# Kernel optimization log

Measured on AMD Instinct MI355X. Metric: run time of the kernel, lower is better.

Reference implementation:

```python
import jax, jax.numpy as jnp
import numpy as np
import math

D_MODEL = 1024
NHEAD = 16
D_K = D_MODEL // NHEAD
SEQ = 2048
BATCH = 2


def setup_inputs() -> dict:
    key = jax.random.key(0)
    ks = jax.random.split(key, 8)
    s = 1.0 / math.sqrt(D_MODEL)
    return {
        "q": jax.random.normal(ks[0], (SEQ, BATCH, D_MODEL), jnp.float32),
        "k": jax.random.normal(ks[1], (SEQ, BATCH, D_MODEL), jnp.float32),
        "v": jax.random.normal(ks[2], (SEQ, BATCH, D_MODEL), jnp.float32),
        "mask": jnp.zeros((1, 1, SEQ, SEQ), jnp.float32),
        "Wq": jax.random.normal(ks[3], (D_MODEL, D_MODEL), jnp.float32) * s,
        "bq": jnp.zeros((D_MODEL,), jnp.float32),
        "Wk": jax.random.normal(ks[4], (D_MODEL, D_MODEL), jnp.float32) * s,
        "bk": jnp.zeros((D_MODEL,), jnp.float32),
        "Wv": jax.random.normal(ks[5], (D_MODEL, D_MODEL), jnp.float32) * s,
        "bv": jnp.zeros((D_MODEL,), jnp.float32),
        "Wo": jax.random.normal(ks[6], (D_MODEL, D_MODEL), jnp.float32) * s,
        "bo": jnp.zeros((D_MODEL,), jnp.float32),
    }


def _split_heads(x):
    # (seq, batch, d_model) -> (batch, nhead, seq, d_k)
    S, B, _ = x.shape
    return x.reshape(S, B, NHEAD, D_K).transpose(1, 2, 0, 3)


def reference(q, k, v, mask, Wq, bq, Wk, bk, Wv, bv, Wo, bo):
    S, B, _ = q.shape
    qh = _split_heads(q @ Wq.T + bq)  # (B, H, S, Dk)
    kh = _split_heads(k @ Wk.T + bk)
    vh = _split_heads(v @ Wv.T + bv)
    scale = 1.0 / math.sqrt(D_K)
    scores = jnp.einsum("bhsd,bhtd->bhst", qh, kh) * scale + mask
    attn = jax.nn.softmax(scores, axis=-1)  # dropout is identity at inference
    out = jnp.einsum("bhst,bhtd->bhsd", attn, vh)  # (B, H, S, Dk)
    # combine heads -> (S, B, d_model), then output projection
    out = out.transpose(2, 0, 1, 3).reshape(S, B, D_MODEL)
    return out @ Wo.T + bo
```

## Files before the change

kernel.cpp:

```cpp
#include <hip/hip_runtime.h>


#define DEV static __device__ __forceinline__

typedef unsigned short u16;
typedef __attribute__((ext_vector_type(8))) short short8;
typedef __attribute__((ext_vector_type(4))) float f32x4;
typedef __attribute__((ext_vector_type(16))) float f32x16;
typedef __attribute__((ext_vector_type(4))) unsigned short ushort4v;
typedef __attribute__((ext_vector_type(4))) unsigned int uint4v;

#define SEQ   2048
#define BATCH 2
#define DM    1024
#define NH    16
#define DKH   64
#define MROWS (SEQ*BATCH)

DEV u16 f2bf(float f) {
  union { float f; unsigned int u; } v; v.f = f;
  unsigned int u = v.u;
  return (u16)((u + 0x7FFFu + ((u >> 16) & 1u)) >> 16);
}

DEV unsigned int cvtpk_bf16(float lo, float hi) {
  unsigned int r;
  asm("v_cvt_pk_bf16_f32 %0, %1, %2" : "=v"(r) : "v"(lo), "v"(hi));
  return r;
}

DEV void permswap(unsigned int& a, unsigned int& b) {
  asm volatile("v_permlane32_swap_b32 %0, %1" : "+v"(a), "+v"(b));
}

#if __has_builtin(__builtin_amdgcn_exp2f)
#define EXP2(x) __builtin_amdgcn_exp2f(x)
#else
#define EXP2(x) exp2f(x)
#endif

DEV void async16(const void* g, void* l) {
  __builtin_amdgcn_global_load_lds(
      (const __attribute__((address_space(1))) unsigned int*)g,
      (__attribute__((address_space(3))) unsigned int*)l, 16, 0, 0);
}

struct CvtArgs {
  const float* s[8];
  u16* d[8];
  int n[8];
  float scale[8];
  int* flag;
};

__global__ __launch_bounds__(256) void cvt_kernel(CvtArgs a) {
  const int t = blockIdx.y;
  const int n = a.n[t];
  const int stride = 1024 * 256 * 4;
  if (t == 7) {
    const float* __restrict__ m = a.s[7];
    int any = 0;
    for (int i = (blockIdx.x * 256 + threadIdx.x) * 4; i < n; i += stride) {
      f32x4 v = *(const f32x4*)&m[i];
      any |= (v[0] != 0.f); any |= (v[1] != 0.f);
      any |= (v[2] != 0.f); any |= (v[3] != 0.f);
    }
    if (any) atomicOr(a.flag, 1);
    return;
  }
  const float* __restrict__ s = a.s[t];
  u16* __restrict__ d = a.d[t];
  const float sc = a.scale[t];
  for (int i = (blockIdx.x * 256 + threadIdx.x) * 4; i < n; i += stride) {
    f32x4 f = *(const f32x4*)&s[i];
    ushort4v o;
    o[0] = f2bf(f[0] * sc); o[1] = f2bf(f[1] * sc);
    o[2] = f2bf(f[2] * sc); o[3] = f2bf(f[3] * sc);
    *(ushort4v*)&d[i] = o;
  }
}

template <int MT, int NT, typename OutT>
DEV void gemm_body(const u16* __restrict__ A,
                   const u16* __restrict__ W,
                   const float* __restrict__ bias, float bscale,
                   OutT* __restrict__ C,
                   u16* As, u16* Bs,
                   int M, int N, int K, int m0, int n0) {
  const int tid = threadIdx.x;
  const int lane = tid & 63;
  const int wid = tid >> 6;
  const int wr = wid >> 1, wc = wid & 1;
  const int sr = lane & 15, g = lane >> 4;

  f32x4 acc[MT][NT] = {};

  const int arow = tid >> 3;
  const int acol = (tid & 7) * 8;
  const size_t abase = (size_t)(m0 + arow) * K + acol;
  const size_t bbase = (size_t)(n0 + arow) * K + acol;

  for (int kt = 0; kt < K; kt += 64) {
#pragma unroll
    for (int j = 0; j < MT; ++j)
      async16(A + abase + (size_t)j * 32 * K + kt, (char*)As + j * 4096 + wid * 1024);
#pragma unroll
    for (int j = 0; j < NT; ++j)
      async16(W + bbase + (size_t)j * 32 * K + kt, (char*)Bs + j * 4096 + wid * 1024);
    __syncthreads();
#pragma unroll
    for (int kk = 0; kk < 2; ++kk) {
      short8 af[MT], bf[NT];
#pragma unroll
      for (int mt = 0; mt < MT; ++mt)
        af[mt] = *(const short8*)&As[(wr * MT * 16 + mt * 16 + sr) * 64 + kk * 32 + g * 8];
#pragma unroll
      for (int nt = 0; nt < NT; ++nt)
        bf[nt] = *(const short8*)&Bs[(wc * NT * 16 + nt * 16 + sr) * 64 + kk * 32 + g * 8];
#pragma unroll
      for (int mt = 0; mt < MT; ++mt)
#pragma unroll
        for (int nt = 0; nt < NT; ++nt)
          acc[mt][nt] = __builtin_amdgcn_mfma_f32_16x16x32_bf16(af[mt], bf[nt], acc[mt][nt], 0, 0, 0);
    }
    __syncthreads();
  }

#pragma unroll
  for (int nt = 0; nt < NT; ++nt) {
    const int col = n0 + wc * NT * 16 + nt * 16 + sr;
    const float bv = bias[col] * bscale;
#pragma unroll
    for (int mt = 0; mt < MT; ++mt) {
#pragma unroll
      for (int r = 0; r < 4; ++r) {
        const int row = m0 + wr * MT * 16 + mt * 16 + g * 4 + r;
        const float val = acc[mt][nt][r] + bv;
        if constexpr (sizeof(OutT) == 2)
          C[(size_t)row * N + col] = f2bf(val);
        else
          C[(size_t)row * N + col] = val;
      }
    }
  }
}

struct GemmPtrs {
  const u16* A[3];
  const u16* W[3];
  const float* bias[3];
  float bscale[3];
  u16* C[3];
};

__global__ __launch_bounds__(256) void gemm_qkv_kernel(GemmPtrs p, int M, int N, int K) {
  __shared__ u16 As[128 * 64];
  __shared__ u16 Bs[128 * 64];
  const int z = blockIdx.z;
  const int fl = blockIdx.x + 32 * blockIdx.y;
  const int virt = (fl & 7) * 32 + (fl >> 3);
  const int mb = virt >> 3, nb = virt & 7;
  gemm_body<4, 4, u16>(p.A[z], p.W[z], p.bias[z], p.bscale[z], p.C[z], As, Bs,
                       M, N, K, mb * 128, nb * 128);
}

__global__ __launch_bounds__(256) void gemm_f32_kernel(const u16* __restrict__ A,
                                                       const u16* __restrict__ W,
                                                       const float* __restrict__ bias,
                                                       float* __restrict__ C,
                                                       int M, int N, int K) {
  __shared__ u16 As[64 * 64];
  __shared__ u16 Bs[128 * 64];
  const int fl = blockIdx.x + 64 * blockIdx.y;
  const int virt = (fl & 7) * 64 + (fl >> 3);
  const int mb = virt >> 3, nb = virt & 7;
  gemm_body<2, 4, float>(A, W, bias, 1.0f, C, As, Bs, M, N, K,
                         mb * 64, nb * 128);
}

__global__ __launch_bounds__(256) void vtrans_kernel(const u16* __restrict__ Vh,
                                                     u16* __restrict__ VT) {
  __shared__ u16 tl[4096];
  const int tid = threadIdx.x;
  const int w = tid >> 6;
  const int t0 = blockIdx.x * 64;
  const int bh = blockIdx.y;
  const int b = bh >> 4, h = bh & 15;
  const int str = tid >> 3;
  const int scc = (tid & 7) * 8;
#pragma unroll
  for (int it = 0; it < 2; ++it)
    async16(Vh + (size_t)((t0 + str + it * 32) * 2 + b) * 1024 + h * 64 + scc,
            (char*)tl + it * 4096 + w * 1024);
  __syncthreads();
  const int dk = tid >> 2;
  const int t4 = (tid & 3) * 16;
  short8 ov[2];
#pragma unroll
  for (int half = 0; half < 2; ++half)
#pragma unroll
    for (int j = 0; j < 8; ++j)
      ov[half][j] = (short)tl[(t4 + half * 8 + j) * 64 + dk];
  u16* dst = VT + (size_t)(bh * 64 + dk) * 2048 + t0 + t4;
  *(short8*)dst = ov[0];
  *(short8*)(dst + 8) = ov[1];
}

__global__ __launch_bounds__(256, 2) void attn7_kernel(const u16* __restrict__ Q,
                                                       const u16* __restrict__ K,
                                                       const u16* __restrict__ VT,
                                                       const float* __restrict__ mask,
                                                       const int* __restrict__ maskflag,
                                                       u16* __restrict__ O) {
  __shared__ u16 Kl[2][4096];
  __shared__ u16 Vl[2][4096];

  const int tid = threadIdx.x;
  const int lane = tid & 63;
  const int w = tid >> 6;
  const int ln = lane & 31;
  const int hi = lane >> 5;
  const int sw = (ln & 7) << 4;

  const int flat = blockIdx.x;
  const int virt = ((flat & 7) << 6) | (flat >> 3);
  const int qi = virt & 15;
  const int bh = virt >> 4;
  const int q0 = qi * 128 + w * 32;
  const int b = bh >> 4, h = bh & 15;
  const int usemask = *maskflag;

  const u16* Qb = Q + b * DM + h * DKH;
  const u16* Kb = K + b * DM + h * DKH;
  const u16* VTb = VT + (size_t)bh * 64 * 2048;

  short8 aq[4];
#pragma unroll
  for (int ks = 0; ks < 4; ++ks)
    aq[ks] = *(const short8*)&Qb[(size_t)(q0 + ln) * 2048 + ks * 16 + hi * 8];

  f32x16 acc[2] = {};
  float l_ = 0.f;
  const float L2E = 1.44269504088896f;

  const int strow = tid >> 3;
  const int scb = (((tid & 7) * 16) ^ ((strow & 7) << 4)) >> 1;

  auto STAGE = [&](int nb, int t0n) {
#pragma unroll
    for (int it = 0; it < 2; ++it) {
      async16(Kb + (size_t)(t0n + strow + it * 32) * 2048 + scb,
              (char*)&Kl[nb][0] + it * 4096 + w * 1024);
      async16(VTb + (size_t)(strow + it * 32) * 2048 + t0n + scb,
              (char*)&Vl[nb][0] + it * 4096 + w * 1024);
    }
  };

  STAGE(0, 0);
  __syncthreads();
  int cur = 0;

  for (int t0 = 0; t0 < SEQ; t0 += 64) {
    if (t0 + 64 < SEQ) STAGE(cur ^ 1, t0 + 64);

    short8 kf[2][4];
#pragma unroll
    for (int tb = 0; tb < 2; ++tb)
#pragma unroll
      for (int ks = 0; ks < 4; ++ks)
        kf[tb][ks] = *(const short8*)((const char*)&Kl[cur][0] +
                                      (tb * 32 + ln) * 128 + ((ks * 32 + hi * 16) ^ sw));

    f32x16 sc[2] = {};
    __builtin_amdgcn_s_setprio(1);
#pragma unroll
    for (int tb = 0; tb < 2; ++tb)
#pragma unroll
      for (int ks = 0; ks < 4; ++ks)
        sc[tb] = __builtin_amdgcn_mfma_f32_32x32x16_bf16(kf[tb][ks], aq[ks], sc[tb], 0, 0, 0);
    __builtin_amdgcn_s_setprio(0);

    short8 vf[2][4];
#pragma unroll
    for (int db = 0; db < 2; ++db)
#pragma unroll
      for (int ks = 0; ks < 4; ++ks)
        vf[db][ks] = *(const short8*)((const char*)&Vl[cur][0] +
                                      (db * 32 + ln) * 128 + ((ks * 32 + hi * 16) ^ sw));

    short8 pa[4];
    float rs = 0.f;
#pragma unroll
    for (int tb = 0; tb < 2; ++tb) {
      float p[16];
#pragma unroll
      for (int r = 0; r < 16; ++r) {
        float xv = sc[tb][r];
        if (usemask)
          xv = __builtin_fmaf(
              mask[(size_t)(q0 + ln) * SEQ + t0 + tb * 32 + (r & 3) + 8 * (r >> 2) + 4 * hi],
              L2E, xv);
        p[r] = EXP2(xv);
        rs += p[r];
      }
#pragma unroll
      for (int ksl = 0; ksl < 2; ++ksl) {
        unsigned int c0 = cvtpk_bf16(p[8 * ksl + 0], p[8 * ksl + 1]);
        unsigned int c1 = cvtpk_bf16(p[8 * ksl + 2], p[8 * ksl + 3]);
        unsigned int c4 = cvtpk_bf16(p[8 * ksl + 4], p[8 * ksl + 5]);
        unsigned int c5 = cvtpk_bf16(p[8 * ksl + 6], p[8 * ksl + 7]);
        permswap(c0, c4);
        permswap(c1, c5);
        union { uint4v u; short8 s; } cc;
        cc.u[0] = c0; cc.u[1] = c1; cc.u[2] = c4; cc.u[3] = c5;
        pa[tb * 2 + ksl] = cc.s;
      }
    }
    l_ += rs;

    __builtin_amdgcn_s_setprio(1);
#pragma unroll
    for (int ks = 0; ks < 4; ++ks)
#pragma unroll
      for (int db = 0; db < 2; ++db)
        acc[db] = __builtin_amdgcn_mfma_f32_32x32x16_bf16(pa[ks], vf[db][ks], acc[db], 0, 0, 0);
    __builtin_amdgcn_s_setprio(0);
    __syncthreads();
    cur ^= 1;
  }

  l_ += __shfl_xor(l_, 32);
  const float linv = 1.f / l_;
  float lb[16];
#pragma unroll
  for (int r = 0; r < 16; ++r)
    lb[r] = __shfl(linv, (r & 3) + 8 * (r >> 2) + 4 * hi);
  const size_t obase = (size_t)b * DM + h * DKH;
#pragma unroll
  for (int db = 0; db < 2; ++db)
#pragma unroll
    for (int r = 0; r < 16; ++r) {
      const int q = q0 + (r & 3) + 8 * (r >> 2) + 4 * hi;
      O[(size_t)q * 2048 + obase + db * 32 + ln] = f2bf(acc[db][r] * lb[r]);
    }
}

extern "C" void kernel_launch(void* const* d_in, const int* in_sizes, int n_in,
                              void* d_out, int out_size, void* d_ws, size_t ws_size,
                              hipStream_t stream) {
  const float* q = (const float*)d_in[0];
  const float* k = (const float*)d_in[1];
  const float* v = (const float*)d_in[2];
  const float* msk = (const float*)d_in[3];
  const float* Wq = (const float*)d_in[4];
  const float* bq = (const float*)d_in[5];
  const float* Wk = (const float*)d_in[6];
  const float* bk = (const float*)d_in[7];
  const float* Wv = (const float*)d_in[8];
  const float* bv = (const float*)d_in[9];
  const float* Wo = (const float*)d_in[10];
  const float* bo = (const float*)d_in[11];
  float* out = (float*)d_out;

  char* ws = (char*)d_ws;
  const size_t SZX = (size_t)MROWS * DM * 2;
  const size_t SZW = (size_t)DM * DM * 2;
  u16* qb  = (u16*)(ws + 0 * SZX);
  u16* kb  = (u16*)(ws + 1 * SZX);
  u16* vb  = (u16*)(ws + 2 * SZX);
  u16* Wqb = (u16*)(ws + 3 * SZX + 0 * SZW);
  u16* Wkb = (u16*)(ws + 3 * SZX + 1 * SZW);
  u16* Wvb = (u16*)(ws + 3 * SZX + 2 * SZW);
  u16* Wob = (u16*)(ws + 3 * SZX + 3 * SZW);
  u16* Qh  = (u16*)(ws + 3 * SZX + 4 * SZW + 0 * SZX);
  u16* Kh  = (u16*)(ws + 3 * SZX + 4 * SZW + 1 * SZX);
  u16* Vh  = (u16*)(ws + 3 * SZX + 4 * SZW + 2 * SZX);
  u16* AO  = (u16*)(ws + 3 * SZX + 4 * SZW + 3 * SZX);
  int* flag = (int*)(ws + 7 * SZX + 4 * SZW);
  u16* VTg = qb;

  hipMemsetAsync(flag, 0, 4, stream);

  const float QS = 0.125f * 1.44269504088896f;

  CvtArgs ca;
  ca.s[0] = q;  ca.d[0] = qb;  ca.n[0] = MROWS * DM; ca.scale[0] = 1.f;
  ca.s[1] = k;  ca.d[1] = kb;  ca.n[1] = MROWS * DM; ca.scale[1] = 1.f;
  ca.s[2] = v;  ca.d[2] = vb;  ca.n[2] = MROWS * DM; ca.scale[2] = 1.f;
  ca.s[3] = Wq; ca.d[3] = Wqb; ca.n[3] = DM * DM;    ca.scale[3] = QS;
  ca.s[4] = Wk; ca.d[4] = Wkb; ca.n[4] = DM * DM;    ca.scale[4] = 1.f;
  ca.s[5] = Wv; ca.d[5] = Wvb; ca.n[5] = DM * DM;    ca.scale[5] = 1.f;
  ca.s[6] = Wo; ca.d[6] = Wob; ca.n[6] = DM * DM;    ca.scale[6] = 1.f;
  ca.s[7] = msk; ca.d[7] = nullptr; ca.n[7] = SEQ * SEQ; ca.scale[7] = 1.f;
  ca.flag = flag;
  cvt_kernel<<<dim3(1024, 8, 1), 256, 0, stream>>>(ca);

  GemmPtrs gp;
  gp.A[0] = qb; gp.W[0] = Wqb; gp.bias[0] = bq; gp.bscale[0] = QS;  gp.C[0] = Qh;
  gp.A[1] = kb; gp.W[1] = Wkb; gp.bias[1] = bk; gp.bscale[1] = 1.f; gp.C[1] = Kh;
  gp.A[2] = vb; gp.W[2] = Wvb; gp.bias[2] = bv; gp.bscale[2] = 1.f; gp.C[2] = Vh;
  gemm_qkv_kernel<<<dim3(32, 8, 3), 256, 0, stream>>>(gp, MROWS, DM, DM);

  vtrans_kernel<<<dim3(32, 32, 1), 256, 0, stream>>>(Vh, VTg);

  attn7_kernel<<<dim3(512, 1, 1), 256, 0, stream>>>(Qh, Kh, VTg, msk, flag, AO);

  gemm_f32_kernel<<<dim3(64, 8, 1), 256, 0, stream>>>(AO, Wob, bo, out, MROWS, DM, DM);
}
```

Baseline: 155.6 us.

## Split attention KV range in two with atomic partial accumulation and normalize pass

The attention kernel now splits each (batch, head, query-tile) job across two halves of the key sequence, launching 1024 blocks instead of 512. It also raises the launch-bounds occupancy hint to 4. Each half atomically adds its unnormalized output and row sums into fp32 buffers, and a new norm kernel divides and converts to bf16. This relies on the existing no-max-rescaling softmax, where partial sums combine additively. The goal is more parallelism to fill the GPU, at the cost of two memsets, a 16MB fp32 atomic write pass and an extra kernel launch.

```diff
diff --git a/kernel.cpp b/kernel.cpp
--- a/kernel.cpp
+++ b/kernel.cpp
@@ -206,12 +206,13 @@
   *(short8*)(dst + 8) = ov[1];
 }
 
-__global__ __launch_bounds__(256, 2) void attn7_kernel(const u16* __restrict__ Q,
+__global__ __launch_bounds__(256, 4) void attn9_kernel(const u16* __restrict__ Q,
                                                        const u16* __restrict__ K,
                                                        const u16* __restrict__ VT,
                                                        const float* __restrict__ mask,
                                                        const int* __restrict__ maskflag,
-                                                       u16* __restrict__ O) {
+                                                       float* __restrict__ Opart,
+                                                       float* __restrict__ lpart) {
   __shared__ u16 Kl[2][4096];
   __shared__ u16 Vl[2][4096];
 
@@ -223,10 +224,12 @@
   const int sw = (ln & 7) << 4;
 
   const int flat = blockIdx.x;
-  const int virt = ((flat & 7) << 6) | (flat >> 3);
+  const int virt = ((flat & 7) << 7) | (flat >> 3);
+  const int bh = virt >> 5;
+  const int half = (virt >> 4) & 1;
   const int qi = virt & 15;
-  const int bh = virt >> 4;
   const int q0 = qi * 128 + w * 32;
+  const int tbase = half * 1024;
   const int b = bh >> 4, h = bh & 15;
   const int usemask = *maskflag;
 
@@ -256,12 +259,12 @@
     }
   };
 
-  STAGE(0, 0);
+  STAGE(0, tbase);
   __syncthreads();
   int cur = 0;
 
-  for (int t0 = 0; t0 < SEQ; t0 += 64) {
-    if (t0 + 64 < SEQ) STAGE(cur ^ 1, t0 + 64);
+  for (int t0 = tbase; t0 < tbase + 1024; t0 += 64) {
+    if (t0 + 64 < tbase + 1024) STAGE(cur ^ 1, t0 + 64);
 
     short8 kf[2][4];
 #pragma unroll
@@ -330,19 +333,31 @@
   }
 
   l_ += __shfl_xor(l_, 32);
-  const float linv = 1.f / l_;
-  float lb[16];
-#pragma unroll
-  for (int r = 0; r < 16; ++r)
-    lb[r] = __shfl(linv, (r & 3) + 8 * (r >> 2) + 4 * hi);
+  if (lane < 32) atomicAdd(&lpart[bh * 2048 + q0 + ln], l_);
   const size_t obase = (size_t)b * DM + h * DKH;
 #pragma unroll
   for (int db = 0; db < 2; ++db)
 #pragma unroll
     for (int r = 0; r < 16; ++r) {
       const int q = q0 + (r & 3) + 8 * (r >> 2) + 4 * hi;
-      O[(size_t)q * 2048 + obase + db * 32 + ln] = f2bf(acc[db][r] * lb[r]);
-    }
+      atomicAdd(&Opart[(size_t)q * 2048 + obase + db * 32 + ln], acc[db][r]);
+    }
+}
+
+__global__ __launch_bounds__(256) void norm_kernel(const float* __restrict__ Opart,
+                                                   const float* __restrict__ lpart,
+                                                   u16* __restrict__ AO) {
+  const int i4 = (blockIdx.x * 256 + threadIdx.x) * 4;
+  const int row = i4 >> 10;
+  const int col = i4 & 1023;
+  const int b = row & 1, q = row >> 1, h = col >> 6;
+  const float l = lpart[(b * 16 + h) * 2048 + q];
+  const float inv = 1.0f / l;
+  f32x4 o = *(const f32x4*)&Opart[i4];
+  ushort4v out;
+  out[0] = f2bf(o[0] * inv); out[1] = f2bf(o[1] * inv);
+  out[2] = f2bf(o[2] * inv); out[3] = f2bf(o[3] * inv);
+  *(ushort4v*)&AO[i4] = out;
 }
 
 extern "C" void kernel_launch(void* const* d_in, const int* in_sizes, int n_in,
@@ -378,6 +393,8 @@
   u16* AO  = (u16*)(ws + 3 * SZX + 4 * SZW + 3 * SZX);
   int* flag = (int*)(ws + 7 * SZX + 4 * SZW);
   u16* VTg = qb;
+  float* Opart = (float*)kb;
+  float* lpart = (float*)Wqb;
 
   hipMemsetAsync(flag, 0, 4, stream);
 
@@ -403,7 +420,12 @@
 
   vtrans_kernel<<<dim3(32, 32, 1), 256, 0, stream>>>(Vh, VTg);
 
-  attn7_kernel<<<dim3(512, 1, 1), 256, 0, stream>>>(Qh, Kh, VTg, msk, flag, AO);
+  hipMemsetAsync(Opart, 0, (size_t)MROWS * DM * 4, stream);
+  hipMemsetAsync(lpart, 0, 32 * 2048 * 4, stream);
+
+  attn9_kernel<<<dim3(1024, 1, 1), 256, 0, stream>>>(Qh, Kh, VTg, msk, flag, Opart, lpart);
+
+  norm_kernel<<<dim3(MROWS * DM / 1024, 1, 1), 256, 0, stream>>>(Opart, lpart, AO);
 
   gemm_f32_kernel<<<dim3(64, 8, 1), 256, 0, stream>>>(AO, Wob, bo, out, MROWS, DM, DM);
 }
```

Result: slower. 193.7 us (+24.5%).
